# Kernel optimization log

Measured on AMD Instinct MI355X. Metric: run time of the kernel, lower is better.

The kernel has to match this reference:

```python
import jax, jax.numpy as jnp
import numpy as np

N_USER = 100000
N_ITEM = 50000
N_NODES = N_USER + N_ITEM
N_EDGES = 2000000
N_LAYERS = 3
EMB = 64
BATCH = 2048


def setup_inputs() -> dict:
    key = jax.random.key(0)
    ks = jax.random.split(key, 7)
    return {
        "user_emb": 0.1 * jax.random.normal(ks[0], (N_USER, EMB), dtype=jnp.float32),
        "item_emb": 0.1 * jax.random.normal(ks[1], (N_ITEM, EMB), dtype=jnp.float32),
        "adj_vals": jax.random.uniform(ks[2], (N_EDGES,), dtype=jnp.float32),
        "adj_rows": jax.random.randint(ks[3], (N_EDGES,), 0, N_NODES, dtype=jnp.int32),
        "adj_cols": jax.random.randint(ks[4], (N_EDGES,), 0, N_NODES, dtype=jnp.int32),
        "users": jax.random.randint(ks[5], (BATCH,), 0, N_USER, dtype=jnp.int32),
        "items": jax.random.randint(ks[6], (BATCH,), 0, N_ITEM, dtype=jnp.int32),
    }


def _computer(user_emb, item_emb, adj_vals, adj_rows, adj_cols):
    # LightGCN propagation: emb_{l+1} = A_hat @ emb_l, output = mean over layers 0..L
    all_emb = jnp.concatenate([user_emb, item_emb], axis=0)  # [N, d]
    emb = all_emb
    acc = all_emb
    for _ in range(N_LAYERS):
        msg = adj_vals[:, None] * emb[adj_cols]              # [E, d]
        emb = jax.ops.segment_sum(msg, adj_rows, num_segments=N_NODES)
        acc = acc + emb
    light_out = acc / jnp.float32(N_LAYERS + 1)              # mean over L+1 embeddings
    return light_out[:N_USER], light_out[N_USER:]


def reference(user_emb, item_emb, adj_vals, adj_rows, adj_cols, users, items):
    all_users, all_items = _computer(user_emb, item_emb, adj_vals, adj_rows, adj_cols)
    u = all_users[users]   # [Bu, d]
    i = all_items[items]   # [Bi, d]
    return jax.nn.sigmoid(u @ i.T)  # [Bu, Bi]
```

## Files before the change

### kernel.cpp

```cpp
#include <hip/hip_runtime.h>
#include <hip/hip_bf16.h>


#define EMB 64
#define NB 512
#define BP 1024

__device__ __forceinline__ float bf2f(unsigned short u) {
    union { unsigned int i; float f; } v;
    v.i = ((unsigned int)u) << 16;
    return v.f;
}
__device__ __forceinline__ unsigned short f2bf(float f) {
    union { float f; unsigned int i; } v;
    v.f = f;
    unsigned int lsb = (v.i >> 16) & 1;
    v.i += 0x7fffu + lsb;
    return (unsigned short)(v.i >> 16);
}

__global__ void ALGN_init_emb(const float4* __restrict__ ue, const float4* __restrict__ ie,
                              ushort4* __restrict__ emb, int nUser4, int n4) {
    int t = blockIdx.x * blockDim.x + threadIdx.x;
    if (t >= n4) return;
    float4 v = (t < nUser4) ? ue[t] : ie[t - nUser4];
    ushort4 o;
    o.x = f2bf(v.x); o.y = f2bf(v.y); o.z = f2bf(v.z); o.w = f2bf(v.w);
    emb[t] = o;
}

__global__ void ALGN_p1(const int* __restrict__ rows, int* __restrict__ blockHist,
                        int nE, int seg, int bsz) {
    __shared__ int h[NB];
    int blk = blockIdx.x;
    for (int i = threadIdx.x; i < NB; i += blockDim.x) h[i] = 0;
    __syncthreads();
    int beg = blk * seg, end = min(beg + seg, nE);
    for (int e = beg + threadIdx.x; e < end; e += blockDim.x)
        atomicAdd(&h[rows[e] / bsz], 1);
    __syncthreads();
    for (int u = threadIdx.x; u < NB; u += blockDim.x)
        blockHist[u * BP + blk] = h[u];
}

__global__ void ALGN_scanA(int* __restrict__ blockHist, int* __restrict__ bucketTotal) {
    __shared__ int tmp[BP];
    int b = blockIdx.x, t = threadIdx.x;
    int v = blockHist[b * BP + t];
    tmp[t] = v;
    __syncthreads();
    for (int off = 1; off < BP; off <<= 1) {
        int x = (t >= off) ? tmp[t - off] : 0;
        __syncthreads();
        tmp[t] += x;
        __syncthreads();
    }
    blockHist[b * BP + t] = tmp[t] - v;
    if (t == BP - 1) bucketTotal[b] = tmp[t];
}

__global__ void ALGN_scanB(const int* __restrict__ bucketTotal, int* __restrict__ bucketBase) {
    __shared__ int tmp[NB];
    int t = threadIdx.x;
    int v = bucketTotal[t];
    tmp[t] = v;
    __syncthreads();
    for (int off = 1; off < NB; off <<= 1) {
        int x = (t >= off) ? tmp[t - off] : 0;
        __syncthreads();
        tmp[t] += x;
        __syncthreads();
    }
    bucketBase[t] = tmp[t] - v;
    if (t == NB - 1) bucketBase[NB] = tmp[t];
}

__global__ void ALGN_p2(const int* __restrict__ rows, const int* __restrict__ cols,
                        const float* __restrict__ vals,
                        const int* __restrict__ blockHist, const int* __restrict__ bucketBase,
                        int2* __restrict__ part, int nE, int seg, int bsz) {
    __shared__ int cur[NB];
    int blk = blockIdx.x;
    for (int u = threadIdx.x; u < NB; u += blockDim.x)
        cur[u] = bucketBase[u] + blockHist[u * BP + blk];
    __syncthreads();
    int beg = blk * seg, end = min(beg + seg, nE);
    for (int e = beg + threadIdx.x; e < end; e += blockDim.x) {
        int r = rows[e];
        int u = r / bsz;
        int pos = atomicAdd(&cur[u], 1);
        int lr = r - u * bsz;
        part[pos] = make_int2((lr << 18) | cols[e], __float_as_int(vals[e]));
    }
}

__global__ void ALGN_bsort(const int2* __restrict__ part, const int* __restrict__ bucketBase,
                           int2* __restrict__ pairs, int* __restrict__ rowPtr,
                           int nNodes, int bsz, int nE) {
    __shared__ int st[NB];
    int b = blockIdx.x, t = threadIdx.x;
    int base = bucketBase[b], lim = bucketBase[b + 1];
    if (t < NB) st[t] = 0;
    __syncthreads();
    for (int j = base + t; j < lim; j += blockDim.x)
        atomicAdd(&st[part[j].x >> 18], 1);
    __syncthreads();
    int v = (t < NB) ? st[t] : 0;
    for (int off = 1; off < NB; off <<= 1) {
        int x = (t >= off && t < NB) ? st[t - off] : 0;
        __syncthreads();
        if (t < NB) st[t] += x;
        __syncthreads();
    }
    int excl = (t < NB) ? st[t] - v : 0;
    __syncthreads();
    if (t < NB) st[t] = excl;
    __syncthreads();
    int row = b * bsz + t;
    if (t < bsz && row < nNodes) rowPtr[row] = base + excl;
    if (b == NB - 1 && t == 0) rowPtr[nNodes] = nE;
    for (int j = base + t; j < lim; j += blockDim.x) {
        int2 p = part[j];
        int lr = p.x >> 18;
        int pos = base + atomicAdd(&st[lr], 1);
        pairs[pos] = make_int2(p.x & 0x3FFFF, p.y);
    }
}

__global__ void ALGN_mark2(const int* __restrict__ rowPtr, const int2* __restrict__ pairs,
                           const int* __restrict__ users, const int* __restrict__ items,
                           int* __restrict__ flag2, int* __restrict__ flagB,
                           int batch, int nUser) {
    int b = blockIdx.x * blockDim.x + threadIdx.x;
    if (b >= 2 * batch) return;
    int row = (b < batch) ? users[b] : (nUser + items[b - batch]);
    flagB[row] = 1;
    flag2[row] = 1;
    int beg = rowPtr[row], end = rowPtr[row + 1];
    for (int j = beg; j < end; ++j) flag2[pairs[j].x] = 1;
}

__device__ __forceinline__ void spmm_row(const ushort4* __restrict__ cur,
                                         ushort4* __restrict__ next,
                                         const int* __restrict__ rowPtr,
                                         const int2* __restrict__ pairs,
                                         int row, int fl) {
    int beg = rowPtr[row];
    int end = rowPtr[row + 1];
    float4 s = make_float4(0.f, 0.f, 0.f, 0.f);
    int j = beg;
    for (; j + 4 <= end; j += 4) {
        int2 e0 = pairs[j + 0];
        int2 e1 = pairs[j + 1];
        int2 e2 = pairs[j + 2];
        int2 e3 = pairs[j + 3];
        ushort4 x0 = cur[(size_t)e0.x * 16 + fl];
        ushort4 x1 = cur[(size_t)e1.x * 16 + fl];
        ushort4 x2 = cur[(size_t)e2.x * 16 + fl];
        ushort4 x3 = cur[(size_t)e3.x * 16 + fl];
        float v0 = __int_as_float(e0.y);
        float v1 = __int_as_float(e1.y);
        float v2 = __int_as_float(e2.y);
        float v3 = __int_as_float(e3.y);
        s.x += v0 * bf2f(x0.x); s.y += v0 * bf2f(x0.y); s.z += v0 * bf2f(x0.z); s.w += v0 * bf2f(x0.w);
        s.x += v1 * bf2f(x1.x); s.y += v1 * bf2f(x1.y); s.z += v1 * bf2f(x1.z); s.w += v1 * bf2f(x1.w);
        s.x += v2 * bf2f(x2.x); s.y += v2 * bf2f(x2.y); s.z += v2 * bf2f(x2.z); s.w += v2 * bf2f(x2.w);
        s.x += v3 * bf2f(x3.x); s.y += v3 * bf2f(x3.y); s.z += v3 * bf2f(x3.z); s.w += v3 * bf2f(x3.w);
    }
    for (; j < end; ++j) {
        int2 e = pairs[j];
        ushort4 x = cur[(size_t)e.x * 16 + fl];
        float v = __int_as_float(e.y);
        s.x += v * bf2f(x.x); s.y += v * bf2f(x.y); s.z += v * bf2f(x.z); s.w += v * bf2f(x.w);
    }
    ushort4 o;
    o.x = f2bf(s.x); o.y = f2bf(s.y); o.z = f2bf(s.z); o.w = f2bf(s.w);
    next[(size_t)row * 16 + fl] = o;
}

__global__ void ALGN_spmm_csr(const ushort4* __restrict__ cur, ushort4* __restrict__ next,
                              const int* __restrict__ rowPtr, const int2* __restrict__ pairs,
                              int nNodes) {
    int tid = blockIdx.x * blockDim.x + threadIdx.x;
    int row = tid >> 4;
    int fl  = tid & 15;
    if (row >= nNodes) return;
    spmm_row(cur, next, rowPtr, pairs, row, fl);
}

__global__ void ALGN_spmm_flag(const ushort4* __restrict__ cur, ushort4* __restrict__ next,
                               const int* __restrict__ rowPtr, const int2* __restrict__ pairs,
                               const int* __restrict__ flag, int nNodes) {
    int tid = blockIdx.x * blockDim.x + threadIdx.x;
    int row = tid >> 4;
    int fl  = tid & 15;
    if (row >= nNodes) return;
    if (!flag[row]) return;
    spmm_row(cur, next, rowPtr, pairs, row, fl);
}

__global__ void ALGN_gather_add(const unsigned short* __restrict__ emb,
                                const int* __restrict__ users, const int* __restrict__ items,
                                float* __restrict__ U, float* __restrict__ I,
                                int batch, int nUser) {
    int t = blockIdx.x * blockDim.x + threadIdx.x;
    if (t >= batch * EMB) return;
    int b = t >> 6, c = t & 63;
    U[t] += bf2f(emb[users[b] * EMB + c]) * 0.25f;
    I[t] += bf2f(emb[(nUser + items[b]) * EMB + c]) * 0.25f;
}

__global__ void ALGN_gemm_sigmoid(const float* __restrict__ U, const float* __restrict__ I,
                                  float* __restrict__ out, int B) {
    __shared__ float su[32][EMB + 1];
    __shared__ float si[32][EMB + 1];
    int tx = threadIdx.x, ty = threadIdx.y;
    int row0 = blockIdx.y * 32, col0 = blockIdx.x * 32;
    int tid = ty * 16 + tx;
    for (int k = tid; k < 32 * EMB; k += 256) {
        int r = k >> 6, c = k & 63;
        su[r][c] = U[(row0 + r) * EMB + c];
        si[r][c] = I[(col0 + r) * EMB + c];
    }
    __syncthreads();
    float s00 = 0.f, s01 = 0.f, s10 = 0.f, s11 = 0.f;
#pragma unroll
    for (int k = 0; k < EMB; ++k) {
        float a0 = su[2 * ty][k],     a1 = su[2 * ty + 1][k];
        float b0 = si[2 * tx][k],     b1 = si[2 * tx + 1][k];
        s00 += a0 * b0; s01 += a0 * b1;
        s10 += a1 * b0; s11 += a1 * b1;
    }
    int r0 = row0 + 2 * ty, c0 = col0 + 2 * tx;
    out[(size_t)r0 * B + c0]           = 1.f / (1.f + __expf(-s00));
    out[(size_t)r0 * B + c0 + 1]       = 1.f / (1.f + __expf(-s01));
    out[(size_t)(r0 + 1) * B + c0]     = 1.f / (1.f + __expf(-s10));
    out[(size_t)(r0 + 1) * B + c0 + 1] = 1.f / (1.f + __expf(-s11));
}

extern "C" void kernel_launch(void* const* d_in, const int* in_sizes, int n_in,
                              void* d_out, int out_size, void* d_ws, size_t ws_size,
                              hipStream_t stream) {
    const float* user_emb = (const float*)d_in[0];
    const float* item_emb = (const float*)d_in[1];
    const float* adj_vals = (const float*)d_in[2];
    const int*   adj_rows = (const int*)d_in[3];
    const int*   adj_cols = (const int*)d_in[4];
    const int*   users    = (const int*)d_in[5];
    const int*   items    = (const int*)d_in[6];
    float* out = (float*)d_out;

    const int nUserF = in_sizes[0];
    const int nItemF = in_sizes[1];
    const int nEdges = in_sizes[2];
    const int batch  = in_sizes[5];
    const int nUser  = nUserF / EMB;
    const int totalF = nUserF + nItemF;
    const int nNodes = totalF / EMB;
    const int n4     = totalF / 4;
    const int bsz    = (nNodes + NB - 1) / NB;
    const int seg    = (nEdges + BP - 1) / BP;

    unsigned short* embA = (unsigned short*)d_ws;
    unsigned short* embB = embA + totalF;
    float* Ub = (float*)(embB + totalF);
    float* Ib = Ub + (size_t)batch * EMB;
    int2*  pairs = (int2*)(Ib + (size_t)batch * EMB);
    int2*  part  = pairs + nEdges;
    int*   rowPtr = (int*)(part + nEdges);
    int*   blockHist   = rowPtr + (nNodes + 1);
    int*   bucketTotal = blockHist + NB * BP;
    int*   bucketBase  = bucketTotal + NB;
    int*   flag2 = bucketBase + (NB + 1);
    int*   flagB = flag2 + nNodes;

    hipMemsetAsync(Ub, 0, (size_t)batch * EMB * sizeof(float) * 2, stream);
    hipMemsetAsync(flag2, 0, (size_t)nNodes * sizeof(int) * 2, stream);

    ALGN_init_emb<<<(n4 + 255) / 256, 256, 0, stream>>>(
        (const float4*)user_emb, (const float4*)item_emb, (ushort4*)embA, nUserF / 4, n4);

    ALGN_p1<<<BP, 256, 0, stream>>>(adj_rows, blockHist, nEdges, seg, bsz);
    ALGN_scanA<<<NB, BP, 0, stream>>>(blockHist, bucketTotal);
    ALGN_scanB<<<1, NB, 0, stream>>>(bucketTotal, bucketBase);
    ALGN_p2<<<BP, 256, 0, stream>>>(adj_rows, adj_cols, adj_vals,
                                    blockHist, bucketBase, part, nEdges, seg, bsz);
    ALGN_bsort<<<NB, 1024, 0, stream>>>(part, bucketBase, pairs, rowPtr, nNodes, bsz, nEdges);

    ALGN_mark2<<<(2 * batch + 255) / 256, 256, 0, stream>>>(
        rowPtr, pairs, users, items, flag2, flagB, batch, nUser);

    ALGN_gather_add<<<(batch * EMB + 255) / 256, 256, 0, stream>>>(
        embA, users, items, Ub, Ib, batch, nUser);

    const int fullBlocks = (nNodes * 16 + 255) / 256;

    ALGN_spmm_csr<<<fullBlocks, 256, 0, stream>>>(
        (const ushort4*)embA, (ushort4*)embB, rowPtr, pairs, nNodes);
    ALGN_gather_add<<<(batch * EMB + 255) / 256, 256, 0, stream>>>(
        embB, users, items, Ub, Ib, batch, nUser);

    ALGN_spmm_flag<<<fullBlocks, 256, 0, stream>>>(
        (const ushort4*)embB, (ushort4*)embA, rowPtr, pairs, flag2, nNodes);
    ALGN_gather_add<<<(batch * EMB + 255) / 256, 256, 0, stream>>>(
        embA, users, items, Ub, Ib, batch, nUser);

    ALGN_spmm_flag<<<fullBlocks, 256, 0, stream>>>(
        (const ushort4*)embA, (ushort4*)embB, rowPtr, pairs, flagB, nNodes);
    ALGN_gather_add<<<(batch * EMB + 255) / 256, 256, 0, stream>>>(
        embB, users, items, Ub, Ib, batch, nUser);

    dim3 gg(batch / 32, batch / 32);
    dim3 gb(16, 16);
    ALGN_gemm_sigmoid<<<gg, gb, 0, stream>>>(Ub, Ib, out, batch);
}
```

Measured before the change: 306.6 us.

## Widen SpMM to 16-byte loads, use wave-shuffle scans, fold memsets into init

SpMM now has each thread handle 8 bf16 features through uint4 loads instead of 4 features through ushort4, which halves the threads per row and doubles the bytes per gather. The three prefix scans switch from shared-memory Hillis-Steele loops with many barriers to wave-level shuffle scans. The two memsets are removed: flag clearing moves into the embedding init kernel, and the first gather writes its values instead of adding. Bucket math uses fixed 512-row buckets with shifts in place of divisions, and mark2 walks neighbour lists with 16 lanes per row. The wider per-thread work may lower occupancy and memory-level parallelism per row, and an unused ALGN_init_emb variant is left behind.

```diff
diff --git a/kernel.cpp b/kernel.cpp
--- a/kernel.cpp
+++ b/kernel.cpp
@@ -3,13 +3,18 @@
 
 
 #define EMB 64
-#define NB 512
+#define BSZ 512
+#define NBMAX 512
 #define BP 1024
 
+__device__ __forceinline__ float bf2f_lo(unsigned int u) {
+    return __int_as_float((int)(u << 16));
+}
+__device__ __forceinline__ float bf2f_hi(unsigned int u) {
+    return __int_as_float((int)(u & 0xFFFF0000u));
+}
 __device__ __forceinline__ float bf2f(unsigned short u) {
-    union { unsigned int i; float f; } v;
-    v.i = ((unsigned int)u) << 16;
-    return v.f;
+    return __int_as_float(((int)u) << 16);
 }
 __device__ __forceinline__ unsigned short f2bf(float f) {
     union { float f; unsigned int i; } v;
@@ -18,107 +23,152 @@
     v.i += 0x7fffu + lsb;
     return (unsigned short)(v.i >> 16);
 }
+__device__ __forceinline__ unsigned int pack2(float a, float b) {
+    return (unsigned int)f2bf(a) | ((unsigned int)f2bf(b) << 16);
+}
+
+__device__ __forceinline__ int wave_iscan(int v) {
+    int lane = threadIdx.x & 63;
+#pragma unroll
+    for (int off = 1; off < 64; off <<= 1) {
+        int x = __shfl_up(v, off, 64);
+        if (lane >= off) v += x;
+    }
+    return v;
+}
 
 __global__ void ALGN_init_emb(const float4* __restrict__ ue, const float4* __restrict__ ie,
-                              ushort4* __restrict__ emb, int nUser4, int n4) {
+                              uint4* __restrict__ emb, int* __restrict__ flags,
+                              int nFlags, int nUser4, int n4) {
     int t = blockIdx.x * blockDim.x + threadIdx.x;
+    if (t < nFlags) flags[t] = 0;
     if (t >= n4) return;
     float4 v = (t < nUser4) ? ue[t] : ie[t - nUser4];
-    ushort4 o;
-    o.x = f2bf(v.x); o.y = f2bf(v.y); o.z = f2bf(v.z); o.w = f2bf(v.w);
+    uint4 o;
+    o.x = pack2(v.x, v.y);
+    o.y = pack2(v.z, v.w);
+    (void)o;
+}
+
+__global__ void ALGN_init_emb8(const float4* __restrict__ ue, const float4* __restrict__ ie,
+                               uint4* __restrict__ emb, int* __restrict__ flags,
+                               int nFlags, int nUser8, int n8) {
+    int t = blockIdx.x * blockDim.x + threadIdx.x;
+    if (t < nFlags) flags[t] = 0;
+    if (t >= n8) return;
+    float4 a, b;
+    if (t < nUser8) { a = ue[2 * t]; b = ue[2 * t + 1]; }
+    else           { a = ie[2 * (t - nUser8)]; b = ie[2 * (t - nUser8) + 1]; }
+    uint4 o;
+    o.x = pack2(a.x, a.y);
+    o.y = pack2(a.z, a.w);
+    o.z = pack2(b.x, b.y);
+    o.w = pack2(b.z, b.w);
     emb[t] = o;
 }
 
 __global__ void ALGN_p1(const int* __restrict__ rows, int* __restrict__ blockHist,
-                        int nE, int seg, int bsz) {
-    __shared__ int h[NB];
+                        int nE, int seg, int nBuckets) {
+    __shared__ int h[NBMAX];
     int blk = blockIdx.x;
-    for (int i = threadIdx.x; i < NB; i += blockDim.x) h[i] = 0;
+    for (int i = threadIdx.x; i < nBuckets; i += blockDim.x) h[i] = 0;
     __syncthreads();
     int beg = blk * seg, end = min(beg + seg, nE);
     for (int e = beg + threadIdx.x; e < end; e += blockDim.x)
-        atomicAdd(&h[rows[e] / bsz], 1);
-    __syncthreads();
-    for (int u = threadIdx.x; u < NB; u += blockDim.x)
+        atomicAdd(&h[rows[e] >> 9], 1);
+    __syncthreads();
+    for (int u = threadIdx.x; u < nBuckets; u += blockDim.x)
         blockHist[u * BP + blk] = h[u];
 }
 
 __global__ void ALGN_scanA(int* __restrict__ blockHist, int* __restrict__ bucketTotal) {
-    __shared__ int tmp[BP];
+    __shared__ int wsum[16];
     int b = blockIdx.x, t = threadIdx.x;
+    int wid = t >> 6;
     int v = blockHist[b * BP + t];
-    tmp[t] = v;
-    __syncthreads();
-    for (int off = 1; off < BP; off <<= 1) {
-        int x = (t >= off) ? tmp[t - off] : 0;
-        __syncthreads();
-        tmp[t] += x;
-        __syncthreads();
-    }
-    blockHist[b * BP + t] = tmp[t] - v;
-    if (t == BP - 1) bucketTotal[b] = tmp[t];
-}
-
-__global__ void ALGN_scanB(const int* __restrict__ bucketTotal, int* __restrict__ bucketBase) {
-    __shared__ int tmp[NB];
+    int isc = wave_iscan(v);
+    if ((t & 63) == 63) wsum[wid] = isc;
+    __syncthreads();
+    if (t < 64) {
+        int s = (t < 16) ? wsum[t] : 0;
+        s = wave_iscan(s);
+        if (t < 16) wsum[t] = s;
+    }
+    __syncthreads();
+    int incl = isc + ((wid > 0) ? wsum[wid - 1] : 0);
+    blockHist[b * BP + t] = incl - v;
+    if (t == BP - 1) bucketTotal[b] = incl;
+}
+
+__global__ void ALGN_scanB(const int* __restrict__ bucketTotal, int* __restrict__ bucketBase,
+                           int nBuckets) {
+    __shared__ int wsum[8];
     int t = threadIdx.x;
-    int v = bucketTotal[t];
-    tmp[t] = v;
-    __syncthreads();
-    for (int off = 1; off < NB; off <<= 1) {
-        int x = (t >= off) ? tmp[t - off] : 0;
-        __syncthreads();
-        tmp[t] += x;
-        __syncthreads();
-    }
-    bucketBase[t] = tmp[t] - v;
-    if (t == NB - 1) bucketBase[NB] = tmp[t];
+    int wid = t >> 6;
+    int v = (t < nBuckets) ? bucketTotal[t] : 0;
+    int isc = wave_iscan(v);
+    if ((t & 63) == 63) wsum[wid] = isc;
+    __syncthreads();
+    if (t < 64) {
+        int s = (t < 8) ? wsum[t] : 0;
+        s = wave_iscan(s);
+        if (t < 8) wsum[t] = s;
+    }
+    __syncthreads();
+    int incl = isc + ((wid > 0) ? wsum[wid - 1] : 0);
+    if (t < nBuckets) bucketBase[t] = incl - v;
+    if (t == nBuckets - 1) bucketBase[nBuckets] = incl;
 }
 
 __global__ void ALGN_p2(const int* __restrict__ rows, const int* __restrict__ cols,
                         const float* __restrict__ vals,
                         const int* __restrict__ blockHist, const int* __restrict__ bucketBase,
-                        int2* __restrict__ part, int nE, int seg, int bsz) {
-    __shared__ int cur[NB];
+                        int2* __restrict__ part, int nE, int seg, int nBuckets) {
+    __shared__ int cur[NBMAX];
     int blk = blockIdx.x;
-    for (int u = threadIdx.x; u < NB; u += blockDim.x)
+    for (int u = threadIdx.x; u < nBuckets; u += blockDim.x)
         cur[u] = bucketBase[u] + blockHist[u * BP + blk];
     __syncthreads();
     int beg = blk * seg, end = min(beg + seg, nE);
     for (int e = beg + threadIdx.x; e < end; e += blockDim.x) {
         int r = rows[e];
-        int u = r / bsz;
+        int u = r >> 9;
         int pos = atomicAdd(&cur[u], 1);
-        int lr = r - u * bsz;
+        int lr = r & 511;
         part[pos] = make_int2((lr << 18) | cols[e], __float_as_int(vals[e]));
     }
 }
 
 __global__ void ALGN_bsort(const int2* __restrict__ part, const int* __restrict__ bucketBase,
                            int2* __restrict__ pairs, int* __restrict__ rowPtr,
-                           int nNodes, int bsz, int nE) {
-    __shared__ int st[NB];
+                           int nNodes, int nBuckets, int nE) {
+    __shared__ int st[BSZ];
+    __shared__ int wsum[8];
     int b = blockIdx.x, t = threadIdx.x;
     int base = bucketBase[b], lim = bucketBase[b + 1];
-    if (t < NB) st[t] = 0;
+    if (t < BSZ) st[t] = 0;
     __syncthreads();
     for (int j = base + t; j < lim; j += blockDim.x)
         atomicAdd(&st[part[j].x >> 18], 1);
     __syncthreads();
-    int v = (t < NB) ? st[t] : 0;
-    for (int off = 1; off < NB; off <<= 1) {
-        int x = (t >= off && t < NB) ? st[t - off] : 0;
-        __syncthreads();
-        if (t < NB) st[t] += x;
-        __syncthreads();
-    }
-    int excl = (t < NB) ? st[t] - v : 0;
-    __syncthreads();
-    if (t < NB) st[t] = excl;
-    __syncthreads();
-    int row = b * bsz + t;
-    if (t < bsz && row < nNodes) rowPtr[row] = base + excl;
-    if (b == NB - 1 && t == 0) rowPtr[nNodes] = nE;
+    int wid = t >> 6;
+    int v = (t < BSZ) ? st[t] : 0;
+    int isc = wave_iscan(v);
+    if ((t & 63) == 63 && wid < 8) wsum[wid] = isc;
+    __syncthreads();
+    if (t < 64) {
+        int s = (t < 8) ? wsum[t] : 0;
+        s = wave_iscan(s);
+        if (t < 8) wsum[t] = s;
+    }
+    __syncthreads();
+    int excl = isc - v + ((wid > 0 && wid < 8) ? wsum[wid - 1] : 0);
+    __syncthreads();
+    if (t < BSZ) st[t] = excl;
+    int row = b * BSZ + t;
+    if (t < BSZ && row < nNodes) rowPtr[row] = base + excl;
+    if (b == nBuckets - 1 && t == 0) rowPtr[nNodes] = nE;
+    __syncthreads();
     for (int j = base + t; j < lim; j += blockDim.x) {
         int2 p = part[j];
         int lr = p.x >> 18;
@@ -131,72 +181,92 @@
                            const int* __restrict__ users, const int* __restrict__ items,
                            int* __restrict__ flag2, int* __restrict__ flagB,
                            int batch, int nUser) {
-    int b = blockIdx.x * blockDim.x + threadIdx.x;
-    if (b >= 2 * batch) return;
-    int row = (b < batch) ? users[b] : (nUser + items[b - batch]);
-    flagB[row] = 1;
-    flag2[row] = 1;
+    int tid = blockIdx.x * blockDim.x + threadIdx.x;
+    int idx = tid >> 4;
+    int ln  = tid & 15;
+    if (idx >= 2 * batch) return;
+    int row = (idx < batch) ? users[idx] : (nUser + items[idx - batch]);
+    if (ln == 0) { flagB[row] = 1; flag2[row] = 1; }
     int beg = rowPtr[row], end = rowPtr[row + 1];
-    for (int j = beg; j < end; ++j) flag2[pairs[j].x] = 1;
-}
-
-__device__ __forceinline__ void spmm_row(const ushort4* __restrict__ cur,
-                                         ushort4* __restrict__ next,
+    for (int j = beg + ln; j < end; j += 16) flag2[pairs[j].x] = 1;
+}
+
+__device__ __forceinline__ void acc8(float& s0, float& s1, float& s2, float& s3,
+                                     float& s4, float& s5, float& s6, float& s7,
+                                     float v, uint4 x) {
+    s0 += v * bf2f_lo(x.x); s1 += v * bf2f_hi(x.x);
+    s2 += v * bf2f_lo(x.y); s3 += v * bf2f_hi(x.y);
+    s4 += v * bf2f_lo(x.z); s5 += v * bf2f_hi(x.z);
+    s6 += v * bf2f_lo(x.w); s7 += v * bf2f_hi(x.w);
+}
+
+__device__ __forceinline__ void spmm_row(const uint4* __restrict__ cur,
+                                         uint4* __restrict__ next,
                                          const int* __restrict__ rowPtr,
                                          const int2* __restrict__ pairs,
                                          int row, int fl) {
     int beg = rowPtr[row];
     int end = rowPtr[row + 1];
-    float4 s = make_float4(0.f, 0.f, 0.f, 0.f);
+    float s0 = 0.f, s1 = 0.f, s2 = 0.f, s3 = 0.f;
+    float s4 = 0.f, s5 = 0.f, s6 = 0.f, s7 = 0.f;
     int j = beg;
     for (; j + 4 <= end; j += 4) {
         int2 e0 = pairs[j + 0];
         int2 e1 = pairs[j + 1];
         int2 e2 = pairs[j + 2];
         int2 e3 = pairs[j + 3];
-        ushort4 x0 = cur[(size_t)e0.x * 16 + fl];
-        ushort4 x1 = cur[(size_t)e1.x * 16 + fl];
-        ushort4 x2 = cur[(size_t)e2.x * 16 + fl];
-        ushort4 x3 = cur[(size_t)e3.x * 16 + fl];
-        float v0 = __int_as_float(e0.y);
-        float v1 = __int_as_float(e1.y);
-        float v2 = __int_as_float(e2.y);
-        float v3 = __int_as_float(e3.y);
-        s.x += v0 * bf2f(x0.x); s.y += v0 * bf2f(x0.y); s.z += v0 * bf2f(x0.z); s.w += v0 * bf2f(x0.w);
-        s.x += v1 * bf2f(x1.x); s.y += v1 * bf2f(x1.y); s.z += v1 * bf2f(x1.z); s.w += v1 * bf2f(x1.w);
-        s.x += v2 * bf2f(x2.x); s.y += v2 * bf2f(x2.y); s.z += v2 * bf2f(x2.z); s.w += v2 * bf2f(x2.w);
-        s.x += v3 * bf2f(x3.x); s.y += v3 * bf2f(x3.y); s.z += v3 * bf2f(x3.z); s.w += v3 * bf2f(x3.w);
+        uint4 x0 = cur[(size_t)e0.x * 8 + fl];
+        uint4 x1 = cur[(size_t)e1.x * 8 + fl];
+        uint4 x2 = cur[(size_t)e2.x * 8 + fl];
+        uint4 x3 = cur[(size_t)e3.x * 8 + fl];
+        acc8(s0, s1, s2, s3, s4, s5, s6, s7, __int_as_float(e0.y), x0);
+        acc8(s0, s1, s2, s3, s4, s5, s6, s7, __int_as_float(e1.y), x1);
+        acc8(s0, s1, s2, s3, s4, s5, s6, s7, __int_as_float(e2.y), x2);
+        acc8(s0, s1, s2, s3, s4, s5, s6, s7, __int_as_float(e3.y), x3);
     }
     for (; j < end; ++j) {
         int2 e = pairs[j];
-        ushort4 x = cur[(size_t)e.x * 16 + fl];
-        float v = __int_as_float(e.y);
-        s.x += v * bf2f(x.x); s.y += v * bf2f(x.y); s.z += v * bf2f(x.z); s.w += v * bf2f(x.w);
-    }
-    ushort4 o;
-    o.x = f2bf(s.x); o.y = f2bf(s.y); o.z = f2bf(s.z); o.w = f2bf(s.w);
-    next[(size_t)row * 16 + fl] = o;
-}
-
-__global__ void ALGN_spmm_csr(const ushort4* __restrict__ cur, ushort4* __restrict__ next,
+        uint4 x = cur[(size_t)e.x * 8 + fl];
+        acc8(s0, s1, s2, s3, s4, s5, s6, s7, __int_as_float(e.y), x);
+    }
+    uint4 o;
+    o.x = pack2(s0, s1);
+    o.y = pack2(s2, s3);
+    o.z = pack2(s4, s5);
+    o.w = pack2(s6, s7);
+    next[(size_t)row * 8 + fl] = o;
+}
+
+__global__ void ALGN_spmm_csr(const uint4* __restrict__ cur, uint4* __restrict__ next,
                               const int* __restrict__ rowPtr, const int2* __restrict__ pairs,
                               int nNodes) {
     int tid = blockIdx.x * blockDim.x + threadIdx.x;
-    int row = tid >> 4;
-    int fl  = tid & 15;
+    int row = tid >> 3;
+    int fl  = tid & 7;
     if (row >= nNodes) return;
     spmm_row(cur, next, rowPtr, pairs, row, fl);
 }
 
-__global__ void ALGN_spmm_flag(const ushort4* __restrict__ cur, ushort4* __restrict__ next,
+__global__ void ALGN_spmm_flag(const uint4* __restrict__ cur, uint4* __restrict__ next,
                                const int* __restrict__ rowPtr, const int2* __restrict__ pairs,
                                const int* __restrict__ flag, int nNodes) {
     int tid = blockIdx.x * blockDim.x + threadIdx.x;
-    int row = tid >> 4;
-    int fl  = tid & 15;
+    int row = tid >> 3;
+    int fl  = tid & 7;
     if (row >= nNodes) return;
     if (!flag[row]) return;
     spmm_row(cur, next, rowPtr, pairs, row, fl);
+}
+
+__global__ void ALGN_gather_set(const unsigned short* __restrict__ emb,
+                                const int* __restrict__ users, const int* __restrict__ items,
+                                float* __restrict__ U, float* __restrict__ I,
+                                int batch, int nUser) {
+    int t = blockIdx.x * blockDim.x + threadIdx.x;
+    if (t >= batch * EMB) return;
+    int b = t >> 6, c = t & 63;
+    U[t] = bf2f(emb[users[b] * EMB + c]) * 0.25f;
+    I[t] = bf2f(emb[(nUser + items[b]) * EMB + c]) * 0.25f;
 }
 
 __global__ void ALGN_gather_add(const unsigned short* __restrict__ emb,
@@ -257,8 +327,8 @@
     const int nUser  = nUserF / EMB;
     const int totalF = nUserF + nItemF;
     const int nNodes = totalF / EMB;
-    const int n4     = totalF / 4;
-    const int bsz    = (nNodes + NB - 1) / NB;
+    const int n8     = totalF / 8;
+    const int nBuckets = (nNodes + BSZ - 1) / BSZ;
     const int seg    = (nEdges + BP - 1) / BP;
 
     unsigned short* embA = (unsigned short*)d_ws;
@@ -269,44 +339,43 @@
     int2*  part  = pairs + nEdges;
     int*   rowPtr = (int*)(part + nEdges);
     int*   blockHist   = rowPtr + (nNodes + 1);
-    int*   bucketTotal = blockHist + NB * BP;
-    int*   bucketBase  = bucketTotal + NB;
-    int*   flag2 = bucketBase + (NB + 1);
+    int*   bucketTotal = blockHist + NBMAX * BP;
+    int*   bucketBase  = bucketTotal + NBMAX;
+    int*   flag2 = bucketBase + (NBMAX + 1);
     int*   flagB = flag2 + nNodes;
 
-    hipMemsetAsync(Ub, 0, (size_t)batch * EMB * sizeof(float) * 2, stream);
-    hipMemsetAsync(flag2, 0, (size_t)nNodes * sizeof(int) * 2, stream);
-
-    ALGN_init_emb<<<(n4 + 255) / 256, 256, 0, stream>>>(
-        (const float4*)user_emb, (const float4*)item_emb, (ushort4*)embA, nUserF / 4, n4);
-
-    ALGN_p1<<<BP, 256, 0, stream>>>(adj_rows, blockHist, nEdges, seg, bsz);
-    ALGN_scanA<<<NB, BP, 0, stream>>>(blockHist, bucketTotal);
-    ALGN_scanB<<<1, NB, 0, stream>>>(bucketTotal, bucketBase);
+    ALGN_init_emb8<<<(n8 + 255) / 256, 256, 0, stream>>>(
+        (const float4*)user_emb, (const float4*)item_emb, (uint4*)embA,
+        flag2, 2 * nNodes, nUserF / 8, n8);
+
+    ALGN_p1<<<BP, 256, 0, stream>>>(adj_rows, blockHist, nEdges, seg, nBuckets);
+    ALGN_scanA<<<nBuckets, BP, 0, stream>>>(blockHist, bucketTotal);
+    ALGN_scanB<<<1, 512, 0, stream>>>(bucketTotal, bucketBase, nBuckets);
     ALGN_p2<<<BP, 256, 0, stream>>>(adj_rows, adj_cols, adj_vals,
-                                    blockHist, bucketBase, part, nEdges, seg, bsz);
-    ALGN_bsort<<<NB, 1024, 0, stream>>>(part, bucketBase, pairs, rowPtr, nNodes, bsz, nEdges);
-
-    ALGN_mark2<<<(2 * batch + 255) / 256, 256, 0, stream>>>(
+                                    blockHist, bucketBase, part, nEdges, seg, nBuckets);
+    ALGN_bsort<<<nBuckets, 1024, 0, stream>>>(part, bucketBase, pairs, rowPtr,
+                                              nNodes, nBuckets, nEdges);
+
+    ALGN_mark2<<<(2 * batch * 16 + 255) / 256, 256, 0, stream>>>(
         rowPtr, pairs, users, items, flag2, flagB, batch, nUser);
 
+    ALGN_gather_set<<<(batch * EMB + 255) / 256, 256, 0, stream>>>(
+        embA, users, items, Ub, Ib, batch, nUser);
+
+    const int fullBlocks = (nNodes * 8 + 255) / 256;
+
+    ALGN_spmm_csr<<<fullBlocks, 256, 0, stream>>>(
+        (const uint4*)embA, (uint4*)embB, rowPtr, pairs, nNodes);
+    ALGN_gather_add<<<(batch * EMB + 255) / 256, 256, 0, stream>>>(
+        embB, users, items, Ub, Ib, batch, nUser);
+
+    ALGN_spmm_flag<<<fullBlocks, 256, 0, stream>>>(
+        (const uint4*)embB, (uint4*)embA, rowPtr, pairs, flag2, nNodes);
     ALGN_gather_add<<<(batch * EMB + 255) / 256, 256, 0, stream>>>(
         embA, users, items, Ub, Ib, batch, nUser);
 
-    const int fullBlocks = (nNodes * 16 + 255) / 256;
-
-    ALGN_spmm_csr<<<fullBlocks, 256, 0, stream>>>(
-        (const ushort4*)embA, (ushort4*)embB, rowPtr, pairs, nNodes);
-    ALGN_gather_add<<<(batch * EMB + 255) / 256, 256, 0, stream>>>(
-        embB, users, items, Ub, Ib, batch, nUser);
-
     ALGN_spmm_flag<<<fullBlocks, 256, 0, stream>>>(
-        (const ushort4*)embB, (ushort4*)embA, rowPtr, pairs, flag2, nNodes);
-    ALGN_gather_add<<<(batch * EMB + 255) / 256, 256, 0, stream>>>(
-        embA, users, items, Ub, Ib, batch, nUser);
-
-    ALGN_spmm_flag<<<fullBlocks, 256, 0, stream>>>(
-        (const ushort4*)embA, (ushort4*)embB, rowPtr, pairs, flagB, nNodes);
+        (const uint4*)embA, (uint4*)embB, rowPtr, pairs, flagB, nNodes);
     ALGN_gather_add<<<(batch * EMB + 255) / 256, 256, 0, stream>>>(
         embB, users, items, Ub, Ib, batch, nUser);
 
```

Measured after the change: 285.3 us. 1.07x faster.
